# Kernel optimization log

Measured on AMD Instinct MI355X. Metric: run time of the kernel, lower is better.

Reference implementation:

```python
import jax, jax.numpy as jnp
import numpy as np

N_U, N_I, E, H = 100000, 50000, 1000000, 128


def setup_inputs() -> dict:
    key = jax.random.key(0)
    ks = jax.random.split(key, 12)
    s = 1.0 / np.sqrt(H)
    return {
        "x_user": jax.random.normal(ks[0], (N_U, H), jnp.float32),
        "x_item": jax.random.normal(ks[1], (N_I, H), jnp.float32),
        "W0": jax.random.normal(ks[2], (H, H), jnp.float32) * s,
        "b0": jnp.zeros((H,), jnp.float32),
        "W1": jax.random.normal(ks[3], (H, H), jnp.float32) * s,
        "b1": jnp.zeros((H,), jnp.float32),
        "W2": jax.random.normal(ks[4], (2 * H, H), jnp.float32) * s,
        "b2": jnp.zeros((H,), jnp.float32),
        "W3": jax.random.normal(ks[5], (2 * H, H), jnp.float32) * s,
        "b3": jnp.zeros((H,), jnp.float32),
        "Wp": jax.random.normal(ks[6], (2 * H, 2), jnp.float32) * s,
        "bp": jnp.zeros((2,), jnp.float32),
        "edge_src": jax.random.randint(ks[7], (E,), 0, N_U, jnp.int32),
        "edge_dst": jax.random.randint(ks[8], (E,), 0, N_I, jnp.int32),
    }


def _inv_sqrt_deg(idx, n):
    # DGL GraphConv: degrees clamped to min 1 before norm
    deg = jax.ops.segment_sum(jnp.ones_like(idx, jnp.float32), idx, num_segments=n)
    return jax.lax.rsqrt(jnp.maximum(deg, 1.0))


def reference(x_user, x_item, W0, b0, W1, b1, W2, b2, W3, b3, Wp, bp,
              edge_src, edge_dst):
    ones_e = None  # degrees computed from edge lists
    inv_du = _inv_sqrt_deg(edge_src, N_U)  # user degree in 'evaluate' edges
    inv_di = _inv_sqrt_deg(edge_dst, N_I)  # item degree in 'evaluate' edges

    # relation 'evaluate' (user -> item), GraphConv(h0, h0), norm='both'
    m_u = x_user * inv_du[:, None]
    agg_item = jax.ops.segment_sum(m_u[edge_src], edge_dst, num_segments=N_I)
    h_item = (agg_item * inv_di[:, None]) @ W0 + b0

    # relation 'evaluated' (item -> user, reversed edges), GraphConv(h1, h1)
    m_i = x_item * inv_di[:, None]
    agg_user = jax.ops.segment_sum(m_i[edge_dst], edge_src, num_segments=N_U)
    h_user = (agg_user * inv_du[:, None]) @ W1 + b1

    h_user = jax.nn.relu(h_user)
    h_item = jax.nn.relu(h_item)

    # concat with inputs, then per-type linear (conv2 / conv3)
    t_user = jnp.concatenate([x_user, h_user], axis=1) @ W2 + b2
    t_item = jnp.concatenate([x_item, h_item], axis=1) @ W3 + b3

    # MLPPredictor over user->item edges: gather-cat-linear
    feat_e = jnp.concatenate([t_user[edge_src], t_item[edge_dst]], axis=1)
    score = feat_e @ Wp + bp
    return jax.nn.softmax(score, axis=1)
```

## Files before the change

kernel.cpp:

```cpp
#include <hip/hip_runtime.h>
#include <hip/hip_bf16.h>


#define H 128
#define CAPU 1536
#define CAPI 3072

typedef __attribute__((ext_vector_type(8))) short bf16x8;
typedef __attribute__((ext_vector_type(4))) float f32x4;

__device__ __forceinline__ unsigned short f2bf(float f) {
    unsigned u = __float_as_uint(f);
    unsigned r = (u + 0x7fffu + ((u >> 16) & 1u)) >> 16;
    return (unsigned short)r;
}
__device__ __forceinline__ float bflo(unsigned b) { return __uint_as_float(b << 16); }
__device__ __forceinline__ float bfhi(unsigned b) { return __uint_as_float(b & 0xffff0000u); }
__device__ __forceinline__ float bfu(unsigned short b) { return __uint_as_float((unsigned)b << 16); }

__global__ __launch_bounds__(256) void k1_prep_p1(
    const float* __restrict__ W0, const float* __restrict__ W1,
    const float* __restrict__ W2, const float* __restrict__ b2,
    const float* __restrict__ W3, const float* __restrict__ b3,
    const float* __restrict__ Wp, const float* __restrict__ bp,
    float* __restrict__ mats,
    unsigned short* __restrict__ WswU, unsigned short* __restrict__ WswI,
    const int* __restrict__ src, const int* __restrict__ dst,
    int* __restrict__ gCurU, int* __restrict__ gCurI,
    unsigned* __restrict__ pairU, unsigned* __restrict__ pairI,
    int E, int nbu, int nbi) {
    __shared__ int cntU[1024], baseU[1024], cntI[512], baseI[512];
    int bx = blockIdx.x;
    if (bx == 0) {
        int tid = threadIdx.x;
        int j = tid >> 1, c = tid & 1;
        float ax = 0.f, ah = 0.f, bx2 = 0.f, bh = 0.f;
        for (int m = 0; m < H; ++m) {
            float wpu = Wp[m * 2 + c];
            float wpi = Wp[(H + m) * 2 + c];
            ax += W2[j * H + m] * wpu;
            ah += W2[(H + j) * H + m] * wpu;
            bx2 += W3[j * H + m] * wpi;
            bh += W3[(H + j) * H + m] * wpi;
        }
        mats[      j * 2 + c] = ax;
        mats[256 + j * 2 + c] = ah;
        mats[512 + j * 2 + c] = bx2;
        mats[768 + j * 2 + c] = bh;
        if (tid < 2) {
            float s1 = 0.f, s2 = 0.f;
            for (int m = 0; m < H; ++m) {
                s1 += b2[m] * Wp[m * 2 + tid];
                s2 += b3[m] * Wp[(H + m) * 2 + tid];
            }
            mats[1024 + tid] = s1 + bp[tid];
            mats[1026 + tid] = s2;
        }
        return;
    }
    if (bx <= 2) {
        const float* W = (bx == 1) ? W0 : W1;
        unsigned short* o = (bx == 1) ? WswU : WswI;
        for (int i = threadIdx.x; i < 4096; i += 256) {
            float4 w = ((const float4*)W)[i];
            int k = i >> 5, n0 = (i & 31) * 4;
            int kb = k >> 3, kj = k & 7;
            o[(kb * 128 + n0 + 0) * 8 + kj] = f2bf(w.x);
            o[(kb * 128 + n0 + 1) * 8 + kj] = f2bf(w.y);
            o[(kb * 128 + n0 + 2) * 8 + kj] = f2bf(w.z);
            o[(kb * 128 + n0 + 3) * 8 + kj] = f2bf(w.w);
        }
        return;
    }
    int t0 = (bx - 3) * 2048;
    for (int i = threadIdx.x; i < nbu; i += 256) cntU[i] = 0;
    for (int i = threadIdx.x; i < nbi; i += 256) cntI[i] = 0;
    __syncthreads();
    #pragma unroll
    for (int j = 0; j < 8; ++j) {
        int e = t0 + j * 256 + threadIdx.x;
        if (e < E) { atomicAdd(&cntU[src[e] >> 7], 1); atomicAdd(&cntI[dst[e] >> 7], 1); }
    }
    __syncthreads();
    for (int i = threadIdx.x; i < nbu; i += 256) {
        int c = cntU[i];
        baseU[i] = c ? (CAPU * i + atomicAdd(&gCurU[i], c)) : 0;
    }
    for (int i = threadIdx.x; i < nbi; i += 256) {
        int c = cntI[i];
        baseI[i] = c ? (CAPI * i + atomicAdd(&gCurI[i], c)) : 0;
    }
    __syncthreads();
    #pragma unroll
    for (int j = 0; j < 8; ++j) {
        int e = t0 + j * 256 + threadIdx.x;
        if (e < E) {
            int s = src[e], d = dst[e];
            int bu = s >> 7, bi = d >> 7;
            int r1 = atomicSub(&cntU[bu], 1) - 1;
            int idx1 = baseU[bu] + r1;
            if (idx1 < CAPU * (bu + 1))
                pairU[idx1] = ((unsigned)(s & 127) << 24) | (unsigned)d;
            int r2 = atomicSub(&cntI[bi], 1) - 1;
            int idx2 = baseI[bi] + r2;
            if (idx2 < CAPI * (bi + 1))
                pairI[idx2] = ((unsigned)(d & 127) << 24) | (unsigned)s;
        }
    }
}

__global__ __launch_bounds__(256) void k2_build_mfma(
    const unsigned* __restrict__ pairU, const unsigned* __restrict__ pairI,
    const int* __restrict__ gCurU, const int* __restrict__ gCurI,
    int2* __restrict__ offU, int2* __restrict__ offI,
    float* __restrict__ invU, float* __restrict__ invI,
    int* __restrict__ valU, int* __restrict__ valI,
    const float* __restrict__ xU, const float* __restrict__ xI,
    const unsigned short* __restrict__ WswU, const unsigned short* __restrict__ WswI,
    unsigned short* __restrict__ yU, unsigned short* __restrict__ yI,
    const float* __restrict__ mats,
    float2* __restrict__ gxU, float2* __restrict__ gxI,
    int NU, int NI, int NBU, int NBI, int shiftU, int shiftI) {
    __shared__ __align__(16) char SMEM[34816];
    int nP2 = NBU + NBI;
    int t = threadIdx.x;

    if (blockIdx.x < (unsigned)nP2) {
        int* cnt  = (int*)SMEM;
        int* pref = cnt + 1024;
        int* part = pref + 1024;
        int* out  = part + 256;
        bool us = blockIdx.x < (unsigned)NBU;
        int b = us ? blockIdx.x : blockIdx.x - NBU;
        const unsigned* pairs = us ? pairU : pairI;
        int cap = us ? CAPU : CAPI;
        int size = us ? gCurU[b] : gCurI[b];
        if (size > cap) size = cap;
        int start = b * cap;
        int shift = us ? shiftU : shiftI;
        int2* off = us ? offU : offI;
        float* inv = us ? invU : invI;
        int* val = us ? valU : valI;
        int n = us ? NU : NI;

        for (int i = t; i < 1024; i += 256) cnt[i] = 0;
        __syncthreads();
        for (int i = t; i < size; i += 256) {
            unsigned p = pairs[start + i];
            int key = (int)((p >> 24) << 3) | (int)((p & 0xFFFFFFu) >> shift);
            atomicAdd(&cnt[key], 1);
        }
        __syncthreads();
        int b4 = t * 4;
        int s0 = cnt[b4], s1 = cnt[b4 + 1], s2 = cnt[b4 + 2], s3 = cnt[b4 + 3];
        int tot = s0 + s1 + s2 + s3;
        part[t] = tot; __syncthreads();
        for (int o2 = 1; o2 < 256; o2 <<= 1) {
            int v = (t >= o2) ? part[t - o2] : 0; __syncthreads();
            part[t] += v; __syncthreads();
        }
        int excl = part[t] - tot;
        pref[b4] = excl;
        pref[b4 + 1] = excl + s0;
        pref[b4 + 2] = excl + s0 + s1;
        pref[b4 + 3] = excl + s0 + s1 + s2;
        __syncthreads();
        if (t < 128) {
            int node = (b << 7) + t;
            if (node < n) {
                int st = pref[t * 8];
                int en = (t == 127) ? size : pref[t * 8 + 8];
                off[node] = make_int2(start + st, start + en);
                inv[node] = rsqrtf(fmaxf((float)(en - st), 1.0f));
            }
        }
        __syncthreads();
        for (int i = t; i < size; i += 256) {
            unsigned p = pairs[start + i];
            int key = (int)((p >> 24) << 3) | (int)((p & 0xFFFFFFu) >> shift);
            int r = atomicAdd(&pref[key], 1);
            out[r] = (int)(p & 0xFFFFFFu);
        }
        __syncthreads();
        for (int i = t; i < size; i += 256) val[start + i] = out[i];
        return;
    }

    unsigned short* As = (unsigned short*)SMEM;
    int mb = blockIdx.x - nP2;
    bool us = mb < NBU;
    int tile = us ? mb : mb - NBU;
    const float* x = us ? xU : xI;
    const unsigned short* Wsw = us ? WswU : WswI;
    unsigned short* y = us ? yU : yI;
    const float* Mx = mats + (us ? 0 : 512);
    const float* cv = mats + (us ? 1024 : 1026);
    float2* gx = us ? gxU : gxI;
    int n = us ? NU : NI;
    int row0 = tile << 7;

    for (int it = 0; it < 16; ++it) {
        int i = it * 256 + t;
        int m = i >> 5, c4 = i & 31;
        int row = row0 + m;
        float4 v = (row < n) ? ((const float4*)x)[(size_t)row * 32 + c4]
                             : make_float4(0.f, 0.f, 0.f, 0.f);
        int k0 = c4 * 4;
        ushort4 s4; s4.x = f2bf(v.x); s4.y = f2bf(v.y); s4.z = f2bf(v.z); s4.w = f2bf(v.w);
        *(ushort4*)&As[((k0 >> 3) * 128 + m) * 8 + (k0 & 7)] = s4;
    }
    __syncthreads();

    int w = t >> 6, l = t & 63;
    int lane15 = l & 15, quad = l >> 4;

    f32x4 acc[2][8];
    #pragma unroll
    for (int rt = 0; rt < 2; ++rt)
        #pragma unroll
        for (int c = 0; c < 8; ++c) acc[rt][c] = (f32x4){0.f, 0.f, 0.f, 0.f};

    #pragma unroll
    for (int ks = 0; ks < 4; ++ks) {
        int kb = ks * 4 + quad;
        bf16x8 a0 = *(const bf16x8*)&As[(kb * 128 + w * 32 + lane15) * 8];
        bf16x8 a1 = *(const bf16x8*)&As[(kb * 128 + w * 32 + 16 + lane15) * 8];
        #pragma unroll
        for (int c = 0; c < 8; ++c) {
            bf16x8 b = *(const bf16x8*)&Wsw[(size_t)(kb * 128 + c * 16 + lane15) * 8];
            acc[0][c] = __builtin_amdgcn_mfma_f32_16x16x32_bf16(a0, b, acc[0][c], 0, 0, 0);
            acc[1][c] = __builtin_amdgcn_mfma_f32_16x16x32_bf16(a1, b, acc[1][c], 0, 0, 0);
        }
    }

    {
        int row = t >> 1, cc = t & 1;
        float p = 0.f;
        for (int kb = 0; kb < 16; ++kb) {
            const unsigned short* ap = &As[(kb * 128 + row) * 8];
            #pragma unroll
            for (int j = 0; j < 8; ++j)
                p += bfu(ap[j]) * Mx[(kb * 8 + j) * 2 + cc];
        }
        int grow = row0 + row;
        if (grow < n) ((float*)&gx[grow])[cc] = p + cv[cc];
    }
    __syncthreads();

    const int LSTR = 136;
    unsigned short* SMu = (unsigned short*)SMEM;
    unsigned short* Lw = SMu + w * 32 * LSTR;
    #pragma unroll
    for (int rt = 0; rt < 2; ++rt) {
        #pragma unroll
        for (int r = 0; r < 4; ++r) {
            int lrow = rt * 16 + quad * 4 + r;
            #pragma unroll
            for (int c = 0; c < 8; ++c)
                Lw[lrow * LSTR + c * 16 + lane15] = f2bf(acc[rt][c][r]);
        }
    }
    #pragma unroll
    for (int pass = 0; pass < 8; ++pass) {
        int lrow = pass * 4 + quad;
        int grow = row0 + w * 32 + lrow;
        uint4 v = *(uint4*)&Lw[lrow * LSTR + lane15 * 8];
        if (grow < n) *(uint4*)&y[(size_t)grow * 128 + lane15 * 8] = v;
    }
}

__global__ __launch_bounds__(256) void gather_kernel(
    const int2* __restrict__ offU, const int* __restrict__ valU,
    const int2* __restrict__ offI, const int* __restrict__ valI,
    const unsigned short* __restrict__ yU, const unsigned short* __restrict__ yI,
    const float* __restrict__ invU, const float* __restrict__ invI,
    const float* __restrict__ b0, const float* __restrict__ b1,
    const float* __restrict__ mats,
    const float2* __restrict__ gxU, const float2* __restrict__ gxI,
    float2* __restrict__ su, float2* __restrict__ si,
    int NU, int NI, int GU) {
    bool us = blockIdx.x < (unsigned)GU;
    int nb = us ? blockIdx.x : blockIdx.x - GU;
    const int2* off = us ? offU : offI;
    const int* val = us ? valU : valI;
    const unsigned short* yo = us ? yI : yU;
    const float* invo = us ? invI : invU;
    const float* inv = us ? invU : invI;
    const float* bv = us ? b1 : b0;
    const float* Mh = mats + (us ? 256 : 768);
    const float2* gx = us ? gxU : gxI;
    float2* so = us ? su : si;
    int n = us ? NU : NI;

    int g = threadIdx.x >> 4, t = threadIdx.x & 15, j0 = t * 8;
    int u = nb * 16 + g;
    if (u >= n) return;

    float a0 = 0, a1 = 0, a2 = 0, a3 = 0, a4 = 0, a5 = 0, a6 = 0, a7 = 0;
    int2 oe = off[u];
    int k = oe.x, end = oe.y;
    for (; k + 4 <= end; k += 4) {
        int v0 = val[k], v1 = val[k + 1], v2 = val[k + 2], v3 = val[k + 3];
        float i0 = invo[v0], i1 = invo[v1], i2 = invo[v2], i3 = invo[v3];
        uint4 w0 = *(const uint4*)(yo + (size_t)v0 * H + j0);
        uint4 w1 = *(const uint4*)(yo + (size_t)v1 * H + j0);
        uint4 w2 = *(const uint4*)(yo + (size_t)v2 * H + j0);
        uint4 w3 = *(const uint4*)(yo + (size_t)v3 * H + j0);
        a0 += bflo(w0.x) * i0 + bflo(w1.x) * i1 + bflo(w2.x) * i2 + bflo(w3.x) * i3;
        a1 += bfhi(w0.x) * i0 + bfhi(w1.x) * i1 + bfhi(w2.x) * i2 + bfhi(w3.x) * i3;
        a2 += bflo(w0.y) * i0 + bflo(w1.y) * i1 + bflo(w2.y) * i2 + bflo(w3.y) * i3;
        a3 += bfhi(w0.y) * i0 + bfhi(w1.y) * i1 + bfhi(w2.y) * i2 + bfhi(w3.y) * i3;
        a4 += bflo(w0.z) * i0 + bflo(w1.z) * i1 + bflo(w2.z) * i2 + bflo(w3.z) * i3;
        a5 += bfhi(w0.z) * i0 + bfhi(w1.z) * i1 + bfhi(w2.z) * i2 + bfhi(w3.z) * i3;
        a6 += bflo(w0.w) * i0 + bflo(w1.w) * i1 + bflo(w2.w) * i2 + bflo(w3.w) * i3;
        a7 += bfhi(w0.w) * i0 + bfhi(w1.w) * i1 + bfhi(w2.w) * i2 + bfhi(w3.w) * i3;
    }
    for (; k < end; ++k) {
        int v0 = val[k];
        float i0 = invo[v0];
        uint4 w0 = *(const uint4*)(yo + (size_t)v0 * H + j0);
        a0 += bflo(w0.x) * i0; a1 += bfhi(w0.x) * i0;
        a2 += bflo(w0.y) * i0; a3 += bfhi(w0.y) * i0;
        a4 += bflo(w0.z) * i0; a5 += bfhi(w0.z) * i0;
        a6 += bflo(w0.w) * i0; a7 += bfhi(w0.w) * i0;
    }
    float iv = inv[u];
    float4 bb0 = *(const float4*)(bv + j0), bb1 = *(const float4*)(bv + j0 + 4);
    float h0 = fmaxf(a0 * iv + bb0.x, 0.f), h1 = fmaxf(a1 * iv + bb0.y, 0.f);
    float h2 = fmaxf(a2 * iv + bb0.z, 0.f), h3 = fmaxf(a3 * iv + bb0.w, 0.f);
    float h4 = fmaxf(a4 * iv + bb1.x, 0.f), h5 = fmaxf(a5 * iv + bb1.y, 0.f);
    float h6 = fmaxf(a6 * iv + bb1.z, 0.f), h7 = fmaxf(a7 * iv + bb1.w, 0.f);
    float4 m0 = *(const float4*)(Mh + j0 * 2),      m1 = *(const float4*)(Mh + j0 * 2 + 4);
    float4 m2 = *(const float4*)(Mh + j0 * 2 + 8),  m3 = *(const float4*)(Mh + j0 * 2 + 12);
    float p0 = h0 * m0.x + h1 * m0.z + h2 * m1.x + h3 * m1.z
             + h4 * m2.x + h5 * m2.z + h6 * m3.x + h7 * m3.z;
    float p1 = h0 * m0.y + h1 * m0.w + h2 * m1.y + h3 * m1.w
             + h4 * m2.y + h5 * m2.w + h6 * m3.y + h7 * m3.w;
    #pragma unroll
    for (int o = 1; o < 16; o <<= 1) { p0 += __shfl_xor(p0, o); p1 += __shfl_xor(p1, o); }
    if (t == 0) {
        float2 gg = gx[u];
        so[u] = make_float2(p0 + gg.x, p1 + gg.y);
    }
}

__global__ void edge_kernel(const int* __restrict__ src, const int* __restrict__ dst,
                            const float2* __restrict__ su, const float2* __restrict__ si,
                            float2* __restrict__ out, int E) {
    int e0 = (blockIdx.x * 256 + threadIdx.x) * 2;
    if (e0 >= E) return;
    int2 s2 = *(const int2*)(src + e0);
    int2 d2 = *(const int2*)(dst + e0);
    float2 a = su[s2.x], b = si[d2.x];
    float l0 = a.x + b.x, l1 = a.y + b.y;
    float m = fmaxf(l0, l1);
    float q0 = __expf(l0 - m), q1 = __expf(l1 - m);
    float r = 1.0f / (q0 + q1);
    out[e0] = make_float2(q0 * r, q1 * r);
    if (e0 + 1 < E) {
        a = su[s2.y]; b = si[d2.y];
        l0 = a.x + b.x; l1 = a.y + b.y;
        m = fmaxf(l0, l1);
        q0 = __expf(l0 - m); q1 = __expf(l1 - m);
        r = 1.0f / (q0 + q1);
        out[e0 + 1] = make_float2(q0 * r, q1 * r);
    }
}

extern "C" void kernel_launch(void* const* d_in, const int* in_sizes, int n_in,
                              void* d_out, int out_size, void* d_ws, size_t ws_size,
                              hipStream_t stream) {
    const float* x_user = (const float*)d_in[0];
    const float* x_item = (const float*)d_in[1];
    const float* W0 = (const float*)d_in[2];
    const float* b0 = (const float*)d_in[3];
    const float* W1 = (const float*)d_in[4];
    const float* b1 = (const float*)d_in[5];
    const float* W2 = (const float*)d_in[6];
    const float* b2 = (const float*)d_in[7];
    const float* W3 = (const float*)d_in[8];
    const float* b3 = (const float*)d_in[9];
    const float* Wp = (const float*)d_in[10];
    const float* bp = (const float*)d_in[11];
    const int* esrc = (const int*)d_in[12];
    const int* edst = (const int*)d_in[13];

    const int NU = in_sizes[0] / H;
    const int NI = in_sizes[1] / H;
    const int E  = in_sizes[12];
    const int NBU = (NU + 127) >> 7;
    const int NBI = (NI + 127) >> 7;
    const int GU = (NU + 15) >> 4, GI = (NI + 15) >> 4;
    auto topshift = [](int n) {
        int bits = 32 - __builtin_clz((unsigned)(n - 1));
        return bits > 3 ? bits - 3 : 0;
    };
    const int shiftU = topshift(NI);
    const int shiftI = topshift(NU);

    auto rnd = [](size_t x) { return (x + 63) & ~(size_t)63; };
    char* base = (char*)d_ws;
    size_t o = 0;
    auto alloc = [&](size_t elems) { void* p = base + o * 4; o += rnd(elems); return p; };

    float* inv_du = (float*)alloc(NU);
    float* inv_di = (float*)alloc(NI);
    float2* su    = (float2*)alloc((size_t)NU * 2);
    float2* si    = (float2*)alloc((size_t)NI * 2);
    float2* gxU   = (float2*)alloc((size_t)NU * 2);
    float2* gxI   = (float2*)alloc((size_t)NI * 2);
    float* mats   = (float*)alloc(1056);
    size_t cur_off = o;
    int* gCurU = (int*)alloc(NBU);
    int* gCurI = (int*)alloc(NBI);
    size_t cur_words = o - cur_off;
    int2* offU = (int2*)alloc((size_t)NU * 2);
    int2* offI = (int2*)alloc((size_t)NI * 2);
    int* valU  = (int*)alloc((size_t)NBU * CAPU);
    int* valI  = (int*)alloc((size_t)NBI * CAPI);
    unsigned* pairU = (unsigned*)alloc((size_t)NBU * CAPU);
    unsigned* pairI = (unsigned*)alloc((size_t)NBI * CAPI);
    unsigned short* WswU = (unsigned short*)alloc(8192);
    unsigned short* WswI = (unsigned short*)alloc(8192);
    unsigned short* yU = (unsigned short*)alloc((size_t)NU * 64);
    unsigned short* yI = (unsigned short*)alloc((size_t)NI * 64);

    hipMemsetAsync(gCurU, 0, cur_words * 4, stream);

    int p1_blocks = (E + 2047) / 2048;
    k1_prep_p1<<<3 + p1_blocks, 256, 0, stream>>>(
        W0, W1, W2, b2, W3, b3, Wp, bp, mats, WswU, WswI,
        esrc, edst, gCurU, gCurI, pairU, pairI, E, NBU, NBI);

    k2_build_mfma<<<2 * (NBU + NBI), 256, 0, stream>>>(
        pairU, pairI, gCurU, gCurI, offU, offI, inv_du, inv_di, valU, valI,
        x_user, x_item, WswU, WswI, yU, yI, mats, gxU, gxI,
        NU, NI, NBU, NBI, shiftU, shiftI);

    gather_kernel<<<GU + GI, 256, 0, stream>>>(
        offU, valU, offI, valI, yU, yI, inv_du, inv_di, b0, b1, mats,
        gxU, gxI, su, si, NU, NI, GU);

    edge_kernel<<<(E / 2 + 255) / 256, 256, 0, stream>>>(esrc, edst, su, si, (float2*)d_out, E);
}
```

Measured before the change: 303.1 us.

## Coarsen CSR build buckets to 512 users / 256 items per chunk

Edge bucketing now groups edges into coarser chunks of 512 user nodes or 256 item nodes with a single capacity, in place of 128-node buckets. The in-block sort keys directly on local node id packed in the upper 12 bits, which removes the two-level key and the shift computation. Per-edge-block work is doubled to 4096 edges, cutting global atomics on bucket cursors and the number of build blocks. The risk is fewer, larger build blocks with more shared-memory staging and less parallelism, plus overflow if a chunk exceeds its capacity.

Measured after the change: 283.3 us. 6.5% less time.

```diff
diff --git a/kernel.cpp b/kernel.cpp
--- a/kernel.cpp
+++ b/kernel.cpp
@@ -3,8 +3,7 @@
 
 
 #define H 128
-#define CAPU 1536
-#define CAPI 3072
+#define CAPC 6656
 
 typedef __attribute__((ext_vector_type(8))) short bf16x8;
 typedef __attribute__((ext_vector_type(4))) float f32x4;
@@ -18,7 +17,7 @@
 __device__ __forceinline__ float bfhi(unsigned b) { return __uint_as_float(b & 0xffff0000u); }
 __device__ __forceinline__ float bfu(unsigned short b) { return __uint_as_float((unsigned)b << 16); }
 
-__global__ __launch_bounds__(256) void k1_prep_p1(
+__global__ __launch_bounds__(256) void k1_prep_pA(
     const float* __restrict__ W0, const float* __restrict__ W1,
     const float* __restrict__ W2, const float* __restrict__ b2,
     const float* __restrict__ W3, const float* __restrict__ b3,
@@ -28,12 +27,11 @@
     const int* __restrict__ src, const int* __restrict__ dst,
     int* __restrict__ gCurU, int* __restrict__ gCurI,
     unsigned* __restrict__ pairU, unsigned* __restrict__ pairI,
-    int E, int nbu, int nbi) {
-    __shared__ int cntU[1024], baseU[1024], cntI[512], baseI[512];
-    int bx = blockIdx.x;
+    int E, int ncu, int nci) {
+    __shared__ int cntU[256], baseU[256], cntI[256], baseI[256];
+    int bx = blockIdx.x, t = threadIdx.x;
     if (bx == 0) {
-        int tid = threadIdx.x;
-        int j = tid >> 1, c = tid & 1;
+        int j = t >> 1, c = t & 1;
         float ax = 0.f, ah = 0.f, bx2 = 0.f, bh = 0.f;
         for (int m = 0; m < H; ++m) {
             float wpu = Wp[m * 2 + c];
@@ -47,21 +45,21 @@
         mats[256 + j * 2 + c] = ah;
         mats[512 + j * 2 + c] = bx2;
         mats[768 + j * 2 + c] = bh;
-        if (tid < 2) {
+        if (t < 2) {
             float s1 = 0.f, s2 = 0.f;
             for (int m = 0; m < H; ++m) {
-                s1 += b2[m] * Wp[m * 2 + tid];
-                s2 += b3[m] * Wp[(H + m) * 2 + tid];
+                s1 += b2[m] * Wp[m * 2 + t];
+                s2 += b3[m] * Wp[(H + m) * 2 + t];
             }
-            mats[1024 + tid] = s1 + bp[tid];
-            mats[1026 + tid] = s2;
+            mats[1024 + t] = s1 + bp[t];
+            mats[1026 + t] = s2;
         }
         return;
     }
     if (bx <= 2) {
         const float* W = (bx == 1) ? W0 : W1;
         unsigned short* o = (bx == 1) ? WswU : WswI;
-        for (int i = threadIdx.x; i < 4096; i += 256) {
+        for (int i = t; i < 4096; i += 256) {
             float4 w = ((const float4*)W)[i];
             int k = i >> 5, n0 = (i & 31) * 4;
             int kb = k >> 3, kj = k & 7;
@@ -72,39 +70,32 @@
         }
         return;
     }
-    int t0 = (bx - 3) * 2048;
-    for (int i = threadIdx.x; i < nbu; i += 256) cntU[i] = 0;
-    for (int i = threadIdx.x; i < nbi; i += 256) cntI[i] = 0;
+    int t0 = (bx - 3) * 4096;
+    cntU[t] = 0; cntI[t] = 0;
     __syncthreads();
     #pragma unroll
-    for (int j = 0; j < 8; ++j) {
-        int e = t0 + j * 256 + threadIdx.x;
-        if (e < E) { atomicAdd(&cntU[src[e] >> 7], 1); atomicAdd(&cntI[dst[e] >> 7], 1); }
+    for (int j = 0; j < 16; ++j) {
+        int e = t0 + j * 256 + t;
+        if (e < E) { atomicAdd(&cntU[src[e] >> 9], 1); atomicAdd(&cntI[dst[e] >> 8], 1); }
     }
     __syncthreads();
-    for (int i = threadIdx.x; i < nbu; i += 256) {
-        int c = cntU[i];
-        baseU[i] = c ? (CAPU * i + atomicAdd(&gCurU[i], c)) : 0;
-    }
-    for (int i = threadIdx.x; i < nbi; i += 256) {
-        int c = cntI[i];
-        baseI[i] = c ? (CAPI * i + atomicAdd(&gCurI[i], c)) : 0;
-    }
+    if (t < ncu) { int c = cntU[t]; baseU[t] = c ? (CAPC * t + atomicAdd(&gCurU[t], c)) : 0; }
+    if (t < nci) { int c = cntI[t]; baseI[t] = c ? (CAPC * t + atomicAdd(&gCurI[t], c)) : 0; }
     __syncthreads();
     #pragma unroll
-    for (int j = 0; j < 8; ++j) {
-        int e = t0 + j * 256 + threadIdx.x;
+    for (int j = 0; j < 16; ++j) {
+        int e = t0 + j * 256 + t;
         if (e < E) {
             int s = src[e], d = dst[e];
-            int bu = s >> 7, bi = d >> 7;
+            int bu = s >> 9, bi = d >> 8;
             int r1 = atomicSub(&cntU[bu], 1) - 1;
-            int idx1 = baseU[bu] + r1;
-            if (idx1 < CAPU * (bu + 1))
-                pairU[idx1] = ((unsigned)(s & 127) << 24) | (unsigned)d;
+            int i1 = baseU[bu] + r1;
+            if (i1 < CAPC * (bu + 1))
+                pairU[i1] = ((unsigned)(s & 511) << 20) | (unsigned)d;
             int r2 = atomicSub(&cntI[bi], 1) - 1;
-            int idx2 = baseI[bi] + r2;
-            if (idx2 < CAPI * (bi + 1))
-                pairI[idx2] = ((unsigned)(d & 127) << 24) | (unsigned)s;
+            int i2 = baseI[bi] + r2;
+            if (i2 < CAPC * (bi + 1))
+                pairI[i2] = ((unsigned)(d & 255) << 20) | (unsigned)s;
         }
     }
 }
@@ -120,74 +111,68 @@
     unsigned short* __restrict__ yU, unsigned short* __restrict__ yI,
     const float* __restrict__ mats,
     float2* __restrict__ gxU, float2* __restrict__ gxI,
-    int NU, int NI, int NBU, int NBI, int shiftU, int shiftI) {
+    int NU, int NI, int ncu, int nci, int NBU, int NBI) {
     __shared__ __align__(16) char SMEM[34816];
-    int nP2 = NBU + NBI;
+    int nPB = ncu + nci;
     int t = threadIdx.x;
 
-    if (blockIdx.x < (unsigned)nP2) {
-        int* cnt  = (int*)SMEM;
-        int* pref = cnt + 1024;
-        int* part = pref + 1024;
-        int* out  = part + 256;
-        bool us = blockIdx.x < (unsigned)NBU;
-        int b = us ? blockIdx.x : blockIdx.x - NBU;
+    if (blockIdx.x < (unsigned)nPB) {
+        bool us = blockIdx.x < (unsigned)ncu;
+        int cb = us ? blockIdx.x : blockIdx.x - ncu;
         const unsigned* pairs = us ? pairU : pairI;
-        int cap = us ? CAPU : CAPI;
-        int size = us ? gCurU[b] : gCurI[b];
-        if (size > cap) size = cap;
-        int start = b * cap;
-        int shift = us ? shiftU : shiftI;
+        int size = us ? gCurU[cb] : gCurI[cb];
+        if (size > CAPC) size = CAPC;
+        int start = cb * CAPC;
+        int nodesPer = us ? 512 : 256;
+        int nodeBase = cb * nodesPer;
+        int n = us ? NU : NI;
         int2* off = us ? offU : offI;
         float* inv = us ? invU : invI;
         int* val = us ? valU : valI;
-        int n = us ? NU : NI;
-
-        for (int i = t; i < 1024; i += 256) cnt[i] = 0;
+
+        int* cnt  = (int*)SMEM;
+        int* pref = cnt + nodesPer;
+        int* part = pref + nodesPer;
+        int* stage = part + 256;
+
+        for (int i = t; i < nodesPer; i += 256) cnt[i] = 0;
+        __syncthreads();
+        for (int i = t; i < size; i += 256) atomicAdd(&cnt[pairs[start + i] >> 20], 1);
+        __syncthreads();
+        int g = nodesPer >> 8;
+        int b0 = t * g;
+        int lv0 = cnt[b0], lv1 = (g == 2) ? cnt[b0 + 1] : 0;
+        int lsum = lv0 + lv1;
+        part[t] = lsum; __syncthreads();
+        for (int o2 = 1; o2 < 256; o2 <<= 1) {
+            int v = (t >= o2) ? part[t - o2] : 0; __syncthreads();
+            part[t] += v; __syncthreads();
+        }
+        int excl = part[t] - lsum;
+        pref[b0] = excl;
+        if (g == 2) pref[b0 + 1] = excl + lv0;
+        __syncthreads();
+        for (int i = t; i < nodesPer; i += 256) {
+            int node = nodeBase + i;
+            if (node < n) {
+                int st = pref[i];
+                off[node] = make_int2(start + st, start + st + cnt[i]);
+                inv[node] = rsqrtf(fmaxf((float)cnt[i], 1.0f));
+            }
+        }
         __syncthreads();
         for (int i = t; i < size; i += 256) {
             unsigned p = pairs[start + i];
-            int key = (int)((p >> 24) << 3) | (int)((p & 0xFFFFFFu) >> shift);
-            atomicAdd(&cnt[key], 1);
+            int r = atomicAdd(&pref[p >> 20], 1);
+            stage[r] = (int)(p & 0xFFFFFu);
         }
         __syncthreads();
-        int b4 = t * 4;
-        int s0 = cnt[b4], s1 = cnt[b4 + 1], s2 = cnt[b4 + 2], s3 = cnt[b4 + 3];
-        int tot = s0 + s1 + s2 + s3;
-        part[t] = tot; __syncthreads();
-        for (int o2 = 1; o2 < 256; o2 <<= 1) {
-            int v = (t >= o2) ? part[t - o2] : 0; __syncthreads();
-            part[t] += v; __syncthreads();
-        }
-        int excl = part[t] - tot;
-        pref[b4] = excl;
-        pref[b4 + 1] = excl + s0;
-        pref[b4 + 2] = excl + s0 + s1;
-        pref[b4 + 3] = excl + s0 + s1 + s2;
-        __syncthreads();
-        if (t < 128) {
-            int node = (b << 7) + t;
-            if (node < n) {
-                int st = pref[t * 8];
-                int en = (t == 127) ? size : pref[t * 8 + 8];
-                off[node] = make_int2(start + st, start + en);
-                inv[node] = rsqrtf(fmaxf((float)(en - st), 1.0f));
-            }
-        }
-        __syncthreads();
-        for (int i = t; i < size; i += 256) {
-            unsigned p = pairs[start + i];
-            int key = (int)((p >> 24) << 3) | (int)((p & 0xFFFFFFu) >> shift);
-            int r = atomicAdd(&pref[key], 1);
-            out[r] = (int)(p & 0xFFFFFFu);
-        }
-        __syncthreads();
-        for (int i = t; i < size; i += 256) val[start + i] = out[i];
+        for (int i = t; i < size; i += 256) val[start + i] = stage[i];
         return;
     }
 
     unsigned short* As = (unsigned short*)SMEM;
-    int mb = blockIdx.x - nP2;
+    int mb = blockIdx.x - nPB;
     bool us = mb < NBU;
     int tile = us ? mb : mb - NBU;
     const float* x = us ? xU : xI;
@@ -388,15 +373,11 @@
     const int NU = in_sizes[0] / H;
     const int NI = in_sizes[1] / H;
     const int E  = in_sizes[12];
+    const int NCU = (NU + 511) >> 9;
+    const int NCI = (NI + 255) >> 8;
     const int NBU = (NU + 127) >> 7;
     const int NBI = (NI + 127) >> 7;
     const int GU = (NU + 15) >> 4, GI = (NI + 15) >> 4;
-    auto topshift = [](int n) {
-        int bits = 32 - __builtin_clz((unsigned)(n - 1));
-        return bits > 3 ? bits - 3 : 0;
-    };
-    const int shiftU = topshift(NI);
-    const int shiftI = topshift(NU);
 
     auto rnd = [](size_t x) { return (x + 63) & ~(size_t)63; };
     char* base = (char*)d_ws;
@@ -411,15 +392,15 @@
     float2* gxI   = (float2*)alloc((size_t)NI * 2);
     float* mats   = (float*)alloc(1056);
     size_t cur_off = o;
-    int* gCurU = (int*)alloc(NBU);
-    int* gCurI = (int*)alloc(NBI);
+    int* gCurU = (int*)alloc(NCU);
+    int* gCurI = (int*)alloc(NCI);
     size_t cur_words = o - cur_off;
     int2* offU = (int2*)alloc((size_t)NU * 2);
     int2* offI = (int2*)alloc((size_t)NI * 2);
-    int* valU  = (int*)alloc((size_t)NBU * CAPU);
-    int* valI  = (int*)alloc((size_t)NBI * CAPI);
-    unsigned* pairU = (unsigned*)alloc((size_t)NBU * CAPU);
-    unsigned* pairI = (unsigned*)alloc((size_t)NBI * CAPI);
+    int* valU  = (int*)alloc((size_t)NCU * CAPC);
+    int* valI  = (int*)alloc((size_t)NCI * CAPC);
+    unsigned* pairU = (unsigned*)alloc((size_t)NCU * CAPC);
+    unsigned* pairI = (unsigned*)alloc((size_t)NCI * CAPC);
     unsigned short* WswU = (unsigned short*)alloc(8192);
     unsigned short* WswI = (unsigned short*)alloc(8192);
     unsigned short* yU = (unsigned short*)alloc((size_t)NU * 64);
@@ -427,15 +408,15 @@
 
     hipMemsetAsync(gCurU, 0, cur_words * 4, stream);
 
-    int p1_blocks = (E + 2047) / 2048;
-    k1_prep_p1<<<3 + p1_blocks, 256, 0, stream>>>(
+    int pa_blocks = (E + 4095) / 4096;
+    k1_prep_pA<<<3 + pa_blocks, 256, 0, stream>>>(
         W0, W1, W2, b2, W3, b3, Wp, bp, mats, WswU, WswI,
-        esrc, edst, gCurU, gCurI, pairU, pairI, E, NBU, NBI);
-
-    k2_build_mfma<<<2 * (NBU + NBI), 256, 0, stream>>>(
+        esrc, edst, gCurU, gCurI, pairU, pairI, E, NCU, NCI);
+
+    k2_build_mfma<<<NCU + NCI + NBU + NBI, 256, 0, stream>>>(
         pairU, pairI, gCurU, gCurI, offU, offI, inv_du, inv_di, valU, valI,
         x_user, x_item, WswU, WswI, yU, yI, mats, gxU, gxI,
-        NU, NI, NBU, NBI, shiftU, shiftI);
+        NU, NI, NCU, NCI, NBU, NBI);
 
     gather_kernel<<<GU + GI, 256, 0, stream>>>(
         offU, valU, offI, valI, yU, yI, inv_du, inv_di, b0, b1, mats,
```
